# Kernel tuning notes

Measured on AMD Instinct MI355X. Metric: run time of the kernel, lower is better.

Reference implementation:

```python
import jax, jax.numpy as jnp
import numpy as np

N_HEADS = 16
EMBED_DIM = 1024

def setup_inputs() -> dict:
    key = jax.random.key(0)
    ks = jax.random.split(key, 5)
    C = EMBED_DIM
    s = 0.02
    return {
        "x": jax.random.normal(ks[0], (4, 2048, C), dtype=jnp.float32),
        "W_attn": jax.random.normal(ks[1], (C, 3 * C), dtype=jnp.float32) * s,
        "b_attn": jnp.zeros((3 * C,), dtype=jnp.float32),
        "W_proj": jax.random.normal(ks[2], (C, C), dtype=jnp.float32) * s,
        "b_proj": jnp.zeros((C,), dtype=jnp.float32),
    }

def reference(x, W_attn, b_attn, W_proj, b_proj):
    B, T, C = x.shape
    H = N_HEADS
    hd = C // H
    qkv = x @ W_attn + b_attn                      # [B,T,3C]
    q, k, v = jnp.split(qkv, 3, axis=-1)
    # [B,T,C] -> [B,H,T,hd]
    q = q.reshape(B, T, H, hd).transpose(0, 2, 1, 3)
    k = k.reshape(B, T, H, hd).transpose(0, 2, 1, 3)
    v = v.reshape(B, T, H, hd).transpose(0, 2, 1, 3)
    scale = 1.0 / np.sqrt(hd).astype(np.float32)
    att = jnp.einsum("bhqd,bhkd->bhqk", q, k) * scale   # [B,H,T,T]
    causal = jnp.tril(jnp.ones((T, T), dtype=bool))
    att = jnp.where(causal[None, None], att, -jnp.inf)
    att = jax.nn.softmax(att, axis=-1)
    y = jnp.einsum("bhqk,bhkd->bhqd", att, v)            # [B,H,T,hd]
    y = y.transpose(0, 2, 1, 3).reshape(B, T, C)
    return y @ W_proj + b_proj
```

## Files before the change

### kernel.cpp

```cpp
#include <hip/hip_runtime.h>
#include <stdint.h>

#define T_ 2048
#define C_ 1024
#define H_ 16
#define HD_ 64

typedef __attribute__((ext_vector_type(8))) short bf16x8;
typedef __attribute__((ext_vector_type(4))) float f32x4;

__device__ __forceinline__ unsigned short f2b(float f) {
  union { float f; unsigned u; } v; v.f = f;
  return (unsigned short)((v.u + 0x7fffu + ((v.u >> 16) & 1u)) >> 16);
}

__global__ void cvt_f32_bf16(const float* __restrict__ in, unsigned short* __restrict__ out, int n4) {
  int stride = gridDim.x * blockDim.x;
  for (int i = blockIdx.x * blockDim.x + threadIdx.x; i < n4; i += stride) {
    float4 v = ((const float4*)in)[i];
    ushort4 o;
    o.x = f2b(v.x); o.y = f2b(v.y); o.z = f2b(v.z); o.w = f2b(v.w);
    ((ushort4*)out)[i] = o;
  }
}

__global__ void transpose_cvt(const float* __restrict__ in, unsigned short* __restrict__ out, int K, int N) {
  __shared__ float tile[32][33];
  int k0 = blockIdx.x * 32, n0 = blockIdx.y * 32;
  int tx = threadIdx.x & 31, ty = threadIdx.x >> 5;
#pragma unroll
  for (int i = 0; i < 4; ++i)
    tile[ty + i*8][tx] = in[(size_t)(k0 + ty + i*8) * N + n0 + tx];
  __syncthreads();
#pragma unroll
  for (int i = 0; i < 4; ++i)
    out[(size_t)(n0 + ty + i*8) * K + k0 + tx] = f2b(tile[tx][ty + i*8]);
}

#define GL16(g, l) __builtin_amdgcn_global_load_lds((const __attribute__((address_space(1))) void*)(g), (__attribute__((address_space(3))) void*)(l), 16, 0, 0)

template<int EPI>
__global__ __launch_bounds__(256) void gemm128(
    const unsigned short* __restrict__ A,
    const unsigned short* __restrict__ Bt,
    const float* __restrict__ bias,
    float* __restrict__ outF,
    unsigned short* __restrict__ outQ,
    unsigned short* __restrict__ outK,
    unsigned short* __restrict__ outV,
    int M, int N, int K)
{
  __shared__ __align__(16) unsigned short Al[2][128*32];
  __shared__ __align__(16) unsigned short Bl[2][128*32];
  const int tid = threadIdx.x, lane = tid & 63, w = tid >> 6;
  const int wm = w >> 1, wn = w & 1;
  const int m0 = blockIdx.x * 128, n0 = blockIdx.y * 128;

  f32x4 acc[4][4];
#pragma unroll
  for (int i = 0; i < 4; ++i)
#pragma unroll
    for (int j = 0; j < 4; ++j)
      acc[i][j] = (f32x4)0.0f;

  const int NT = K >> 5;
  const int srow = lane >> 2;
  const int punit = lane & 3;

#pragma unroll
  for (int i = 0; i < 2; ++i) {
    int chunk = w*2 + i;
    int row = chunk*16 + srow;
    int lu = punit ^ ((row >> 1) & 3);
    GL16(A  + (size_t)(m0 + row) * K + lu*8, &Al[0][chunk*512]);
    GL16(Bt + (size_t)(n0 + row) * K + lu*8, &Bl[0][chunk*512]);
  }
  __syncthreads();

  for (int kt = 0; kt < NT; ++kt) {
    if (kt + 1 < NT) {
      int nb = (kt+1) & 1;
#pragma unroll
      for (int i = 0; i < 2; ++i) {
        int chunk = w*2 + i;
        int row = chunk*16 + srow;
        int lu = punit ^ ((row >> 1) & 3);
        GL16(A  + (size_t)(m0 + row) * K + ((kt+1) << 5) + lu*8, &Al[nb][chunk*512]);
        GL16(Bt + (size_t)(n0 + row) * K + ((kt+1) << 5) + lu*8, &Bl[nb][chunk*512]);
      }
    }
    {
      const int cb = kt & 1;
      const int r16 = lane & 15, u = lane >> 4;
      bf16x8 af[4], bfr[4];
#pragma unroll
      for (int f = 0; f < 4; ++f) {
        int ra = wm*64 + f*16 + r16;
        af[f]  = *(const bf16x8*)&Al[cb][ra*32 + ((u ^ ((ra>>1)&3)) << 3)];
        int rb = wn*64 + f*16 + r16;
        bfr[f] = *(const bf16x8*)&Bl[cb][rb*32 + ((u ^ ((rb>>1)&3)) << 3)];
      }
#pragma unroll
      for (int i = 0; i < 4; ++i)
#pragma unroll
        for (int j = 0; j < 4; ++j)
          acc[i][j] = __builtin_amdgcn_mfma_f32_16x16x32_bf16(af[i], bfr[j], acc[i][j], 0, 0, 0);
    }
    __syncthreads();
  }

  const int u = lane >> 4, r16 = lane & 15;
#pragma unroll
  for (int i = 0; i < 4; ++i) {
    int rbase = m0 + wm*64 + i*16 + u*4;
#pragma unroll
    for (int j = 0; j < 4; ++j) {
      int col = n0 + wn*64 + j*16 + r16;
      float bv = bias[col];
      if (EPI == 0) {
#pragma unroll
        for (int r = 0; r < 4; ++r)
          outF[(size_t)(rbase + r) * N + col] = acc[i][j][r] + bv;
      } else {
        int sec = col >> 10, c = col & 1023, h = c >> 6, d = c & 63;
        int b = rbase >> 11, t = rbase & (T_ - 1);
        if (sec == 0) {
#pragma unroll
          for (int r = 0; r < 4; ++r)
            outQ[(((size_t)b*H_ + h)*T_ + (t + r))*HD_ + d] = f2b((acc[i][j][r] + bv) * 0.125f);
        } else if (sec == 1) {
#pragma unroll
          for (int r = 0; r < 4; ++r)
            outK[(((size_t)b*H_ + h)*T_ + (t + r))*HD_ + d] = f2b(acc[i][j][r] + bv);
        } else {
          ushort4 pk;
          pk.x = f2b(acc[i][j][0] + bv);
          pk.y = f2b(acc[i][j][1] + bv);
          pk.z = f2b(acc[i][j][2] + bv);
          pk.w = f2b(acc[i][j][3] + bv);
          *(ushort4*)&outV[(((size_t)b*H_ + h)*HD_ + d)*T_ + t] = pk;
        }
      }
    }
  }
}

__global__ __launch_bounds__(256) void attn_fused(
    const unsigned short* __restrict__ Q,
    const unsigned short* __restrict__ Kc,
    const unsigned short* __restrict__ Vt,
    unsigned short* __restrict__ Y)
{
  __shared__ __align__(16) unsigned short Kl[64*64];
  __shared__ __align__(16) unsigned short Vl[64*64];
  __shared__ __align__(16) unsigned short Pl[4][32*64];
  const int tid = threadIdx.x, lane = tid & 63, w = tid >> 6;
  const int r16 = lane & 15, u = lane >> 4;
  const int q0 = blockIdx.x * 128;
  const int bh = blockIdx.y;
  const int b = bh >> 4, h = bh & 15;
  const int qw = q0 + w*32;

  const unsigned short* Qb = Q  + ((size_t)bh*T_ + qw)*HD_;
  const unsigned short* Kb = Kc + (size_t)bh*T_*HD_;
  const unsigned short* Vb = Vt + (size_t)bh*HD_*T_;

  bf16x8 qf[2][2];
#pragma unroll
  for (int fm = 0; fm < 2; ++fm)
#pragma unroll
    for (int kk = 0; kk < 2; ++kk)
      qf[fm][kk] = *(const bf16x8*)&Qb[(size_t)(fm*16 + r16)*HD_ + kk*32 + u*8];

  f32x4 o[2][4];
  float mr[2][4], lr[2][4];
#pragma unroll
  for (int fm = 0; fm < 2; ++fm) {
#pragma unroll
    for (int fd = 0; fd < 4; ++fd) o[fm][fd] = (f32x4)0.0f;
#pragma unroll
    for (int jr = 0; jr < 4; ++jr) { mr[fm][jr] = -1e30f; lr[fm][jr] = 0.0f; }
  }

  const int ntiles = (q0 >> 6) + 2;

  bf16x8 kr[2], vr[2], kr2[2], vr2[2];
#pragma unroll
  for (int p = 0; p < 2; ++p) {
    int idx = p*256 + tid;
    int row = idx >> 3, un = idx & 7;
    kr[p] = *(const bf16x8*)&Kb[(size_t)row*HD_ + un*8];
    vr[p] = *(const bf16x8*)&Vb[(size_t)row*T_ + un*8];
  }
#pragma unroll
  for (int p = 0; p < 2; ++p) {
    int idx = p*256 + tid;
    int row = idx >> 3, un = idx & 7;
    int wu = un ^ (row & 7);
    *(bf16x8*)&Kl[row*64 + wu*8] = kr[p];
    *(bf16x8*)&Vl[row*64 + wu*8] = vr[p];
  }
  __syncthreads();

  for (int t = 0; t < ntiles; ++t) {
    const int kv0 = t * 64;
    const bool pre = (t + 1 < ntiles);
    if (pre) {
      const int kvn = kv0 + 64;
#pragma unroll
      for (int p = 0; p < 2; ++p) {
        int idx = p*256 + tid;
        int row = idx >> 3, un = idx & 7;
        kr2[p] = *(const bf16x8*)&Kb[(size_t)(kvn + row)*HD_ + un*8];
        vr2[p] = *(const bf16x8*)&Vb[(size_t)row*T_ + kvn + un*8];
      }
    }
    if (kv0 <= qw + 31) {
      f32x4 s[2][4];
#pragma unroll
      for (int fm = 0; fm < 2; ++fm)
#pragma unroll
        for (int fn = 0; fn < 4; ++fn) s[fm][fn] = (f32x4)0.0f;
#pragma unroll
      for (int fn = 0; fn < 4; ++fn) {
        int rk = fn*16 + r16;
#pragma unroll
        for (int kk = 0; kk < 2; ++kk) {
          int un = (kk*4 + u) ^ (rk & 7);
          bf16x8 kf = *(const bf16x8*)&Kl[rk*64 + un*8];
          s[0][fn] = __builtin_amdgcn_mfma_f32_16x16x32_bf16(qf[0][kk], kf, s[0][fn], 0,0,0);
          s[1][fn] = __builtin_amdgcn_mfma_f32_16x16x32_bf16(qf[1][kk], kf, s[1][fn], 0,0,0);
        }
      }
      if (kv0 + 63 > qw) {
#pragma unroll
        for (int fm = 0; fm < 2; ++fm)
#pragma unroll
          for (int fn = 0; fn < 4; ++fn) {
            int kv = kv0 + fn*16 + r16;
#pragma unroll
            for (int jr = 0; jr < 4; ++jr) {
              int q = qw + fm*16 + u*4 + jr;
              if (kv > q) s[fm][fn][jr] = -1e30f;
            }
          }
      }
      float mt[2][4];
#pragma unroll
      for (int fm = 0; fm < 2; ++fm)
#pragma unroll
        for (int jr = 0; jr < 4; ++jr)
          mt[fm][jr] = fmaxf(fmaxf(s[fm][0][jr], s[fm][1][jr]), fmaxf(s[fm][2][jr], s[fm][3][jr]));
#pragma unroll
      for (int msk = 1; msk < 16; msk <<= 1)
#pragma unroll
        for (int fm = 0; fm < 2; ++fm)
#pragma unroll
          for (int jr = 0; jr < 4; ++jr)
            mt[fm][jr] = fmaxf(mt[fm][jr], __shfl_xor(mt[fm][jr], msk, 64));
      float alpha[2][4], rs[2][4];
#pragma unroll
      for (int fm = 0; fm < 2; ++fm)
#pragma unroll
        for (int jr = 0; jr < 4; ++jr) {
          float mn = fmaxf(mr[fm][jr], mt[fm][jr]);
          alpha[fm][jr] = __expf(mr[fm][jr] - mn);
          mr[fm][jr] = mn;
          rs[fm][jr] = 0.0f;
        }
#pragma unroll
      for (int fm = 0; fm < 2; ++fm)
#pragma unroll
        for (int fn = 0; fn < 4; ++fn) {
          int kvc = fn*16 + r16;
#pragma unroll
          for (int jr = 0; jr < 4; ++jr) {
            float p = __expf(s[fm][fn][jr] - mr[fm][jr]);
            rs[fm][jr] += p;
            int qloc = fm*16 + u*4 + jr;
            int boff = qloc*128 + ((kvc*2) ^ ((qloc & 7) << 4));
            *(unsigned short*)((char*)&Pl[w][0] + boff) = f2b(p);
          }
        }
#pragma unroll
      for (int msk = 1; msk < 16; msk <<= 1)
#pragma unroll
        for (int fm = 0; fm < 2; ++fm)
#pragma unroll
          for (int jr = 0; jr < 4; ++jr)
            rs[fm][jr] += __shfl_xor(rs[fm][jr], msk, 64);
#pragma unroll
      for (int fm = 0; fm < 2; ++fm)
#pragma unroll
        for (int jr = 0; jr < 4; ++jr)
          lr[fm][jr] = lr[fm][jr]*alpha[fm][jr] + rs[fm][jr];
#pragma unroll
      for (int fm = 0; fm < 2; ++fm)
#pragma unroll
        for (int fd = 0; fd < 4; ++fd)
#pragma unroll
          for (int jr = 0; jr < 4; ++jr)
            o[fm][fd][jr] *= alpha[fm][jr];
#pragma unroll
      for (int kks = 0; kks < 2; ++kks) {
        bf16x8 pa[2];
#pragma unroll
        for (int fm = 0; fm < 2; ++fm) {
          int rq = fm*16 + r16;
          int un = (kks*4 + u) ^ (rq & 7);
          pa[fm] = *(const bf16x8*)&Pl[w][rq*64 + un*8];
        }
#pragma unroll
        for (int fd = 0; fd < 4; ++fd) {
          int rv = fd*16 + r16;
          int un = (kks*4 + u) ^ (rv & 7);
          bf16x8 vf = *(const bf16x8*)&Vl[rv*64 + un*8];
          o[0][fd] = __builtin_amdgcn_mfma_f32_16x16x32_bf16(pa[0], vf, o[0][fd], 0,0,0);
          o[1][fd] = __builtin_amdgcn_mfma_f32_16x16x32_bf16(pa[1], vf, o[1][fd], 0,0,0);
        }
      }
    }
    __syncthreads();
    if (pre) {
#pragma unroll
      for (int p = 0; p < 2; ++p) {
        int idx = p*256 + tid;
        int row = idx >> 3, un = idx & 7;
        int wu = un ^ (row & 7);
        *(bf16x8*)&Kl[row*64 + wu*8] = kr2[p];
        *(bf16x8*)&Vl[row*64 + wu*8] = vr2[p];
      }
      __syncthreads();
    }
  }

#pragma unroll
  for (int fm = 0; fm < 2; ++fm) {
    int tb = qw + fm*16 + u*4;
#pragma unroll
    for (int jr = 0; jr < 4; ++jr) {
      float inv = 1.0f / lr[fm][jr];
      int tt = tb + jr;
#pragma unroll
      for (int fd = 0; fd < 4; ++fd) {
        int c = h*64 + fd*16 + r16;
        Y[((size_t)b*T_ + tt)*C_ + c] = f2b(o[fm][fd][jr] * inv);
      }
    }
  }
}

extern "C" void kernel_launch(void* const* d_in, const int* in_sizes, int n_in,
                              void* d_out, int out_size, void* d_ws, size_t ws_size,
                              hipStream_t stream) {
  const float* x      = (const float*)d_in[0];
  const float* W_attn = (const float*)d_in[1];
  const float* b_attn = (const float*)d_in[2];
  const float* W_proj = (const float*)d_in[3];
  const float* b_proj = (const float*)d_in[4];
  float* out = (float*)d_out;

  char* ws = (char*)d_ws;
  unsigned short* xb  = (unsigned short*)(ws);
  unsigned short* Wta = (unsigned short*)(ws + (16u << 20));
  unsigned short* Wtp = (unsigned short*)(ws + (22u << 20));
  unsigned short* qb  = (unsigned short*)(ws + (24u << 20));
  unsigned short* kb  = (unsigned short*)(ws + (40u << 20));
  unsigned short* vtb = (unsigned short*)(ws + (56u << 20));

  cvt_f32_bf16<<<2048, 256, 0, stream>>>(x, xb, (4 * T_ * C_) / 4);
  transpose_cvt<<<dim3(C_/32, (3*C_)/32), 256, 0, stream>>>(W_attn, Wta, C_, 3*C_);
  transpose_cvt<<<dim3(C_/32, C_/32), 256, 0, stream>>>(W_proj, Wtp, C_, C_);
  gemm128<1><<<dim3(64, 24), 256, 0, stream>>>(xb, Wta, b_attn, nullptr, qb, kb, vtb, 8192, 3072, 1024);
  attn_fused<<<dim3(T_/128, 64), 256, 0, stream>>>(qb, kb, vtb, xb);
  gemm128<0><<<dim3(64, 8), 256, 0, stream>>>(xb, Wtp, b_proj, out, nullptr, nullptr, nullptr, 8192, 1024, 1024);
}
```

Before: 403.2 us.

## Drop shared-memory K/V staging, use exp2 softmax, and remap attention blocks per XCD

The attention kernel no longer stages K and V tiles in shared memory behind block barriers. Each wave reads its K and V fragments straight from global memory, which relies on L2 hits, and stops at its own causal limit instead of the block's. The softmax scale now folds log2(e) into Q so the kernel can call the hardware exp2. A 1D grid remaps blocks so each XCD works on the same (batch, head) set, and pairs long and short query tiles to balance load. Per-wave global loads may raise memory latency and traffic in exchange for removing the barriers.

```diff
diff --git a/kernel.cpp b/kernel.cpp
--- a/kernel.cpp
+++ b/kernel.cpp
@@ -8,6 +8,8 @@
 
 typedef __attribute__((ext_vector_type(8))) short bf16x8;
 typedef __attribute__((ext_vector_type(4))) float f32x4;
+
+#define EXP2F(x) __builtin_amdgcn_exp2f(x)
 
 __device__ __forceinline__ unsigned short f2b(float f) {
   union { float f; unsigned u; } v; v.f = f;
@@ -127,7 +129,7 @@
         if (sec == 0) {
 #pragma unroll
           for (int r = 0; r < 4; ++r)
-            outQ[(((size_t)b*H_ + h)*T_ + (t + r))*HD_ + d] = f2b((acc[i][j][r] + bv) * 0.125f);
+            outQ[(((size_t)b*H_ + h)*T_ + (t + r))*HD_ + d] = f2b((acc[i][j][r] + bv) * 0.18033688f);
         } else if (sec == 1) {
 #pragma unroll
           for (int r = 0; r < 4; ++r)
@@ -151,15 +153,18 @@
     const unsigned short* __restrict__ Vt,
     unsigned short* __restrict__ Y)
 {
-  __shared__ __align__(16) unsigned short Kl[64*64];
-  __shared__ __align__(16) unsigned short Vl[64*64];
   __shared__ __align__(16) unsigned short Pl[4][32*64];
   const int tid = threadIdx.x, lane = tid & 63, w = tid >> 6;
   const int r16 = lane & 15, u = lane >> 4;
-  const int q0 = blockIdx.x * 128;
-  const int bh = blockIdx.y;
+
+  const int l = blockIdx.x;
+  const int xcd = l & 7, slot = l >> 3;
+  const int xr = slot & 15, grp = slot >> 4;
+  const int qtile = (xr & 1) ? (xr >> 1) : (15 - (xr >> 1));
+  const int bh = xcd + grp * 8;
+  const int q0 = qtile * 128;
   const int b = bh >> 4, h = bh & 15;
-  const int qw = q0 + w*32;
+  const int qw = q0 + w * 32;
 
   const unsigned short* Qb = Q  + ((size_t)bh*T_ + qw)*HD_;
   const unsigned short* Kb = Kc + (size_t)bh*T_*HD_;
@@ -182,155 +187,109 @@
     for (int jr = 0; jr < 4; ++jr) { mr[fm][jr] = -1e30f; lr[fm][jr] = 0.0f; }
   }
 
-  const int ntiles = (q0 >> 6) + 2;
-
-  bf16x8 kr[2], vr[2], kr2[2], vr2[2];
-#pragma unroll
-  for (int p = 0; p < 2; ++p) {
-    int idx = p*256 + tid;
-    int row = idx >> 3, un = idx & 7;
-    kr[p] = *(const bf16x8*)&Kb[(size_t)row*HD_ + un*8];
-    vr[p] = *(const bf16x8*)&Vb[(size_t)row*T_ + un*8];
-  }
-#pragma unroll
-  for (int p = 0; p < 2; ++p) {
-    int idx = p*256 + tid;
-    int row = idx >> 3, un = idx & 7;
-    int wu = un ^ (row & 7);
-    *(bf16x8*)&Kl[row*64 + wu*8] = kr[p];
-    *(bf16x8*)&Vl[row*64 + wu*8] = vr[p];
-  }
-  __syncthreads();
+  const int ntiles = (qw >> 6) + 1;
 
   for (int t = 0; t < ntiles; ++t) {
     const int kv0 = t * 64;
-    const bool pre = (t + 1 < ntiles);
-    if (pre) {
-      const int kvn = kv0 + 64;
-#pragma unroll
-      for (int p = 0; p < 2; ++p) {
-        int idx = p*256 + tid;
-        int row = idx >> 3, un = idx & 7;
-        kr2[p] = *(const bf16x8*)&Kb[(size_t)(kvn + row)*HD_ + un*8];
-        vr2[p] = *(const bf16x8*)&Vb[(size_t)row*T_ + kvn + un*8];
-      }
-    }
-    if (kv0 <= qw + 31) {
-      f32x4 s[2][4];
+    f32x4 s[2][4];
+#pragma unroll
+    for (int fm = 0; fm < 2; ++fm)
+#pragma unroll
+      for (int fn = 0; fn < 4; ++fn) s[fm][fn] = (f32x4)0.0f;
+#pragma unroll
+    for (int fn = 0; fn < 4; ++fn) {
+      const size_t krow = (size_t)(kv0 + fn*16 + r16) * HD_;
+#pragma unroll
+      for (int kk = 0; kk < 2; ++kk) {
+        bf16x8 kf = *(const bf16x8*)&Kb[krow + kk*32 + u*8];
+        s[0][fn] = __builtin_amdgcn_mfma_f32_16x16x32_bf16(qf[0][kk], kf, s[0][fn], 0,0,0);
+        s[1][fn] = __builtin_amdgcn_mfma_f32_16x16x32_bf16(qf[1][kk], kf, s[1][fn], 0,0,0);
+      }
+    }
+    if (kv0 + 63 > qw) {
 #pragma unroll
       for (int fm = 0; fm < 2; ++fm)
 #pragma unroll
-        for (int fn = 0; fn < 4; ++fn) s[fm][fn] = (f32x4)0.0f;
-#pragma unroll
-      for (int fn = 0; fn < 4; ++fn) {
-        int rk = fn*16 + r16;
-#pragma unroll
-        for (int kk = 0; kk < 2; ++kk) {
-          int un = (kk*4 + u) ^ (rk & 7);
-          bf16x8 kf = *(const bf16x8*)&Kl[rk*64 + un*8];
-          s[0][fn] = __builtin_amdgcn_mfma_f32_16x16x32_bf16(qf[0][kk], kf, s[0][fn], 0,0,0);
-          s[1][fn] = __builtin_amdgcn_mfma_f32_16x16x32_bf16(qf[1][kk], kf, s[1][fn], 0,0,0);
-        }
-      }
-      if (kv0 + 63 > qw) {
-#pragma unroll
-        for (int fm = 0; fm < 2; ++fm)
-#pragma unroll
-          for (int fn = 0; fn < 4; ++fn) {
-            int kv = kv0 + fn*16 + r16;
-#pragma unroll
-            for (int jr = 0; jr < 4; ++jr) {
-              int q = qw + fm*16 + u*4 + jr;
-              if (kv > q) s[fm][fn][jr] = -1e30f;
-            }
-          }
-      }
-      float mt[2][4];
-#pragma unroll
-      for (int fm = 0; fm < 2; ++fm)
-#pragma unroll
-        for (int jr = 0; jr < 4; ++jr)
-          mt[fm][jr] = fmaxf(fmaxf(s[fm][0][jr], s[fm][1][jr]), fmaxf(s[fm][2][jr], s[fm][3][jr]));
-#pragma unroll
-      for (int msk = 1; msk < 16; msk <<= 1)
-#pragma unroll
-        for (int fm = 0; fm < 2; ++fm)
-#pragma unroll
-          for (int jr = 0; jr < 4; ++jr)
-            mt[fm][jr] = fmaxf(mt[fm][jr], __shfl_xor(mt[fm][jr], msk, 64));
-      float alpha[2][4], rs[2][4];
-#pragma unroll
-      for (int fm = 0; fm < 2; ++fm)
-#pragma unroll
-        for (int jr = 0; jr < 4; ++jr) {
-          float mn = fmaxf(mr[fm][jr], mt[fm][jr]);
-          alpha[fm][jr] = __expf(mr[fm][jr] - mn);
-          mr[fm][jr] = mn;
-          rs[fm][jr] = 0.0f;
-        }
-#pragma unroll
-      for (int fm = 0; fm < 2; ++fm)
-#pragma unroll
         for (int fn = 0; fn < 4; ++fn) {
-          int kvc = fn*16 + r16;
+          int kv = kv0 + fn*16 + r16;
 #pragma unroll
           for (int jr = 0; jr < 4; ++jr) {
-            float p = __expf(s[fm][fn][jr] - mr[fm][jr]);
-            rs[fm][jr] += p;
-            int qloc = fm*16 + u*4 + jr;
-            int boff = qloc*128 + ((kvc*2) ^ ((qloc & 7) << 4));
-            *(unsigned short*)((char*)&Pl[w][0] + boff) = f2b(p);
+            int q = qw + fm*16 + u*4 + jr;
+            if (kv > q) s[fm][fn][jr] = -1e30f;
           }
         }
-#pragma unroll
-      for (int msk = 1; msk < 16; msk <<= 1)
-#pragma unroll
-        for (int fm = 0; fm < 2; ++fm)
-#pragma unroll
-          for (int jr = 0; jr < 4; ++jr)
-            rs[fm][jr] += __shfl_xor(rs[fm][jr], msk, 64);
+    }
+    float mt[2][4];
+#pragma unroll
+    for (int fm = 0; fm < 2; ++fm)
+#pragma unroll
+      for (int jr = 0; jr < 4; ++jr)
+        mt[fm][jr] = fmaxf(fmaxf(s[fm][0][jr], s[fm][1][jr]), fmaxf(s[fm][2][jr], s[fm][3][jr]));
+#pragma unroll
+    for (int msk = 1; msk < 16; msk <<= 1)
 #pragma unroll
       for (int fm = 0; fm < 2; ++fm)
 #pragma unroll
         for (int jr = 0; jr < 4; ++jr)
-          lr[fm][jr] = lr[fm][jr]*alpha[fm][jr] + rs[fm][jr];
+          mt[fm][jr] = fmaxf(mt[fm][jr], __shfl_xor(mt[fm][jr], msk, 64));
+    float alpha[2][4], rs[2][4];
+#pragma unroll
+    for (int fm = 0; fm < 2; ++fm)
+#pragma unroll
+      for (int jr = 0; jr < 4; ++jr) {
+        float mn = fmaxf(mr[fm][jr], mt[fm][jr]);
+        alpha[fm][jr] = EXP2F(mr[fm][jr] - mn);
+        mr[fm][jr] = mn;
+        rs[fm][jr] = 0.0f;
+      }
+#pragma unroll
+    for (int fm = 0; fm < 2; ++fm)
+#pragma unroll
+      for (int fn = 0; fn < 4; ++fn) {
+        int kvc = fn*16 + r16;
+#pragma unroll
+        for (int jr = 0; jr < 4; ++jr) {
+          float p = EXP2F(s[fm][fn][jr] - mr[fm][jr]);
+          rs[fm][jr] += p;
+          int qloc = fm*16 + u*4 + jr;
+          int boff = qloc*128 + ((kvc*2) ^ ((qloc & 7) << 4));
+          *(unsigned short*)((char*)&Pl[w][0] + boff) = f2b(p);
+        }
+      }
+#pragma unroll
+    for (int msk = 1; msk < 16; msk <<= 1)
 #pragma unroll
       for (int fm = 0; fm < 2; ++fm)
 #pragma unroll
-        for (int fd = 0; fd < 4; ++fd)
-#pragma unroll
-          for (int jr = 0; jr < 4; ++jr)
-            o[fm][fd][jr] *= alpha[fm][jr];
-#pragma unroll
-      for (int kks = 0; kks < 2; ++kks) {
-        bf16x8 pa[2];
-#pragma unroll
-        for (int fm = 0; fm < 2; ++fm) {
-          int rq = fm*16 + r16;
-          int un = (kks*4 + u) ^ (rq & 7);
-          pa[fm] = *(const bf16x8*)&Pl[w][rq*64 + un*8];
-        }
-#pragma unroll
-        for (int fd = 0; fd < 4; ++fd) {
-          int rv = fd*16 + r16;
-          int un = (kks*4 + u) ^ (rv & 7);
-          bf16x8 vf = *(const bf16x8*)&Vl[rv*64 + un*8];
-          o[0][fd] = __builtin_amdgcn_mfma_f32_16x16x32_bf16(pa[0], vf, o[0][fd], 0,0,0);
-          o[1][fd] = __builtin_amdgcn_mfma_f32_16x16x32_bf16(pa[1], vf, o[1][fd], 0,0,0);
-        }
-      }
-    }
-    __syncthreads();
-    if (pre) {
-#pragma unroll
-      for (int p = 0; p < 2; ++p) {
-        int idx = p*256 + tid;
-        int row = idx >> 3, un = idx & 7;
-        int wu = un ^ (row & 7);
-        *(bf16x8*)&Kl[row*64 + wu*8] = kr2[p];
-        *(bf16x8*)&Vl[row*64 + wu*8] = vr2[p];
-      }
-      __syncthreads();
+        for (int jr = 0; jr < 4; ++jr)
+          rs[fm][jr] += __shfl_xor(rs[fm][jr], msk, 64);
+#pragma unroll
+    for (int fm = 0; fm < 2; ++fm)
+#pragma unroll
+      for (int jr = 0; jr < 4; ++jr)
+        lr[fm][jr] = lr[fm][jr]*alpha[fm][jr] + rs[fm][jr];
+#pragma unroll
+    for (int fm = 0; fm < 2; ++fm)
+#pragma unroll
+      for (int fd = 0; fd < 4; ++fd)
+#pragma unroll
+        for (int jr = 0; jr < 4; ++jr)
+          o[fm][fd][jr] *= alpha[fm][jr];
+#pragma unroll
+    for (int kks = 0; kks < 2; ++kks) {
+      bf16x8 pa[2];
+#pragma unroll
+      for (int fm = 0; fm < 2; ++fm) {
+        int rq = fm*16 + r16;
+        int un = (kks*4 + u) ^ (rq & 7);
+        pa[fm] = *(const bf16x8*)&Pl[w][rq*64 + un*8];
+      }
+#pragma unroll
+      for (int fd = 0; fd < 4; ++fd) {
+        bf16x8 vf = *(const bf16x8*)&Vb[(size_t)(fd*16 + r16)*T_ + kv0 + kks*32 + u*8];
+        o[0][fd] = __builtin_amdgcn_mfma_f32_16x16x32_bf16(pa[0], vf, o[0][fd], 0,0,0);
+        o[1][fd] = __builtin_amdgcn_mfma_f32_16x16x32_bf16(pa[1], vf, o[1][fd], 0,0,0);
+      }
     }
   }
 
@@ -372,6 +331,6 @@
   transpose_cvt<<<dim3(C_/32, (3*C_)/32), 256, 0, stream>>>(W_attn, Wta, C_, 3*C_);
   transpose_cvt<<<dim3(C_/32, C_/32), 256, 0, stream>>>(W_proj, Wtp, C_, C_);
   gemm128<1><<<dim3(64, 24), 256, 0, stream>>>(xb, Wta, b_attn, nullptr, qb, kb, vtb, 8192, 3072, 1024);
-  attn_fused<<<dim3(T_/128, 64), 256, 0, stream>>>(qb, kb, vtb, xb);
+  attn_fused<<<1024, 256, 0, stream>>>(qb, kb, vtb, xb);
   gemm128<0><<<dim3(64, 8), 256, 0, stream>>>(xb, Wtp, b_proj, out, nullptr, nullptr, nullptr, 8192, 1024, 1024);
 }
```

New measurement: 411.0 us. No clear change (+1.9%).
